# Kernel tuning notes

Measured on AMD Instinct MI355X. Metric: run time of the kernel, lower is better.

Reference implementation:

```python
import jax, jax.numpy as jnp
import numpy as np

TAU_RC = 0.02
TAU_REF = 0.002
V_TH = 1.0
EPS = 1e-7


def lif_rate(I):
    # LIF firing-rate nonlinearity: r = 1/(tau_ref - tau_rc*log1p(-v_th/I)) for I > v_th+eps else 0
    good = I > V_TH + EPS
    safe_I = jnp.where(good, I, V_TH + 1.0)  # avoid log1p of invalid values
    r = 1.0 / (TAU_REF - TAU_RC * jnp.log1p(-V_TH / safe_I))
    return jnp.where(good, r, 0.0)


def setup_inputs() -> dict:
    key = jax.random.key(0)
    kq, kk, kv, ke, kg, kb = jax.random.split(key, 6)
    B, H, T, D = 2, 16, 2048, 64
    block_size = 2048
    Q = jax.random.normal(kq, (B, H, T, D), dtype=jnp.float32)
    K = jax.random.normal(kk, (B, H, T, D), dtype=jnp.float32)
    V = jax.random.normal(kv, (B, H, T, D), dtype=jnp.float32)
    enc = jax.random.normal(ke, (H, block_size, D), dtype=jnp.float32)
    # F.normalize(enc, dim=-1, eps=1e-8): x / max(||x||, eps)
    norm = jnp.maximum(jnp.linalg.norm(enc, axis=-1, keepdims=True), 1e-8)
    enc_hat = enc / norm
    gain = jax.random.uniform(kg, (1, H, block_size, 1), dtype=jnp.float32) * 200.0
    bias = jax.random.uniform(kb, (1, H, block_size, 1), dtype=jnp.float32)
    return {"Q": Q, "K": K, "V": V, "enc_hat": enc_hat, "gain": gain, "bias": bias}


def reference(Q, K, V, enc_hat, gain, bias):
    B, H, T, D = Q.shape
    temperature = jnp.asarray(D ** 0.5, dtype=Q.dtype)
    E = enc_hat[:, :T, :]          # [H, T, D]
    G = gain[:, :, :T, :]          # [1, H, T, 1]
    BIAS = bias[:, :, :T, :]       # [1, H, T, 1]
    # scores against fixed encoders (K is unused, matching the original module)
    I = G * jnp.einsum('bhtd,hsd->bhts', Q, E) + BIAS   # [B, H, T, T]
    scores = lif_rate(I) / temperature
    causal = jnp.tril(jnp.ones((T, T), dtype=bool))[None, None]
    scores = jnp.where(causal, scores, -jnp.inf)
    attn = jax.nn.softmax(scores, axis=-1)
    return jnp.einsum('bhts,bhsd->bhtd', attn, V)
```

## Files before the change

### kernel.cpp

```cpp
#include <hip/hip_runtime.h>
#include <hip/hip_bf16.h>
#include <math.h>

constexpr int Bb = 2, Hh = 16, Tt = 2048;

typedef __attribute__((ext_vector_type(8))) _Float16 f16x8;
typedef __attribute__((ext_vector_type(8))) short bf16x8;
typedef __attribute__((ext_vector_type(4))) float f32x4;
typedef __attribute__((ext_vector_type(16))) float f32x16;
typedef __attribute__((ext_vector_type(4))) unsigned int u32x4;
typedef unsigned int u32;

__device__ __forceinline__ short f2bf(float x){ __hip_bfloat16 h = __float2bfloat16(x); return *(short*)&h; }
__device__ __forceinline__ int swze(int row, int e){ return row*64 + ((((e>>3) ^ (row&7))<<3) | (e&7)); }
__device__ __forceinline__ int swzg(int row, int e0){ return row*64 + ((((e0>>3) ^ (row&7))<<3)); }

__device__ __forceinline__ void gll16(const void* g, void* l){
  __builtin_amdgcn_global_load_lds((const __attribute__((address_space(1))) u32*)g,
                                   (__attribute__((address_space(3))) u32*)l, 16, 0, 0);
}
__device__ __forceinline__ u32 cvtpk(float lo, float hi){
  u32 d; asm("v_cvt_pk_bf16_f32 %0, %1, %2" : "=v"(d) : "v"(lo), "v"(hi)); return d;
}

__global__ __launch_bounds__(256) void prep_e(const float* __restrict__ E, char* __restrict__ Eimg){
  const float* src = E + (size_t)blockIdx.x * 4096;
  char* dst = Eimg + (size_t)blockIdx.x * 16384;
#pragma unroll
  for (int i = 0; i < 2; ++i) {
    const int gid = threadIdx.x + 256 * i;
    const int row = gid >> 3, gc = gid & 7;
    const float* s8 = src + row * 64 + gc * 8;
    float4 a = *(const float4*)s8;
    float4 c = *(const float4*)(s8 + 4);
    float v[8] = {a.x, a.y, a.z, a.w, c.x, c.y, c.z, c.w};
    f16x8 hv, lv;
#pragma unroll
    for (int k = 0; k < 8; ++k) {
      _Float16 hi = (_Float16)v[k];
      hv[k] = hi; lv[k] = (_Float16)(v[k] - (float)hi);
    }
    const int off = row * 128 + ((gc ^ (row & 7)) << 4);
    *(f16x8*)(dst + off) = hv;
    *(f16x8*)(dst + 8192 + off) = lv;
  }
}

__global__ __launch_bounds__(256) void prep_v(const float* __restrict__ V, char* __restrict__ Vimg){
  __shared__ __align__(16) short Tl[64 * 64];
  const int tid = threadIdx.x;
  const int j = blockIdx.x & 31, bh = blockIdx.x >> 5;
  const int s0 = j * 64;
  {
    const int r = tid >> 2, c0 = (tid & 3) * 16;
    const float* src = V + ((size_t)bh * Tt + s0 + r) * 64 + c0;
#pragma unroll
    for (int i = 0; i < 4; ++i) {
      float4 t4 = ((const float4*)src)[i];
      float vv[4] = {t4.x, t4.y, t4.z, t4.w};
#pragma unroll
      for (int k = 0; k < 4; ++k) Tl[swze(c0 + 4 * i + k, r)] = f2bf(vv[k]);
    }
  }
  __syncthreads();
  {
    const int d = tid >> 2, sg = (tid & 3) * 16;
    bf16x8 a = *(const bf16x8*)&Tl[swzg(d, sg)];
    bf16x8 b = *(const bf16x8*)&Tl[swzg(d, sg + 8)];
    char* dst = Vimg + (size_t)blockIdx.x * 8192 + d * 128;
    *(bf16x8*)(dst + ((((sg >> 3) + 0) ^ (d & 7)) << 4)) = a;
    *(bf16x8*)(dst + ((((sg >> 3) + 1) ^ (d & 7)) << 4)) = b;
  }
}

__global__ __launch_bounds__(256, 3) void lif_attn6(
    const float* __restrict__ Q, const float* __restrict__ gain, const float* __restrict__ bias,
    const char* __restrict__ Eimg, const char* __restrict__ Vimg, float* __restrict__ out)
{
  __shared__ __align__(16) char Eb[2][16384];
  __shared__ __align__(16) char Vb[2][8192];
  __shared__ __align__(16) float LsS[128];

  const int tid = threadIdx.x, lane = tid & 63;
  const int l31 = lane & 31, hi2 = lane >> 5;
  const int w = tid >> 6, wc = w & 1, wr = w >> 1;
  const int bh = blockIdx.x & 31, tb = 31 - (blockIdx.x >> 5);
  const int b = bh >> 4, h = bh & 15, t0 = tb * 64;
  const int tg = t0 + 32 * wc + l31;

  const char* etile = Eimg + (size_t)(h * 32) * 16384;
  const char* vtile = Vimg + (size_t)(bh * 32) * 8192;

  f16x8 qh[4], ql[4];
  {
    const float* qp = Q + ((size_t)(b * Hh + h) * Tt + tg) * 64 + 8 * hi2;
#pragma unroll
    for (int kk = 0; kk < 4; ++kk) {
      const float* p0 = qp + 16 * kk;
      float4 a = *(const float4*)p0;
      float4 c = *(const float4*)(p0 + 4);
      float v[8] = {a.x, a.y, a.z, a.w, c.x, c.y, c.z, c.w};
#pragma unroll
      for (int k = 0; k < 8; ++k) {
        _Float16 hi = (_Float16)v[k];
        qh[kk][k] = hi; ql[kk][k] = (_Float16)(v[k] - (float)hi);
      }
    }
  }
  const float gt = gain[h * Tt + tg], bt = bias[h * Tt + tg];

  const int rS = 32 * wr + l31;
  const int eB = rS * 128 + ((hi2 ^ (rS & 7)) << 4);
  const int vB0 = l31 * 128 + (((4 * wr + hi2) ^ (l31 & 7)) << 4);
  const int vB1 = (32 + l31) * 128 + (((4 * wr + hi2) ^ (l31 & 7)) << 4);

  f32x16 oacc0 = 0.f, oacc1 = 0.f;
  float lsum = 0.f;

  {
    const char* g = etile + tid * 16;
#pragma unroll
    for (int c2 = 0; c2 < 4; ++c2) gll16(g + c2 * 4096, &Eb[0][0] + tid * 16 + c2 * 4096);
    const char* gv = vtile + tid * 16;
#pragma unroll
    for (int c2 = 0; c2 < 2; ++c2) gll16(gv + c2 * 4096, &Vb[0][0] + tid * 16 + c2 * 4096);
  }
  __syncthreads();

  int cur = 0;
  for (int j = 0; ; ++j) {
    if (j < tb) {
      const char* g = etile + (size_t)(j + 1) * 16384 + tid * 16;
      char* l = &Eb[cur ^ 1][0] + tid * 16;
#pragma unroll
      for (int c2 = 0; c2 < 4; ++c2) gll16(g + c2 * 4096, l + c2 * 4096);
      const char* gv = vtile + (size_t)(j + 1) * 8192 + tid * 16;
      char* lv = &Vb[cur ^ 1][0] + tid * 16;
#pragma unroll
      for (int c2 = 0; c2 < 2; ++c2) gll16(gv + c2 * 4096, lv + c2 * 4096);
    }
    const char* ec = &Eb[cur][0];
    f32x16 sacc = 0.f;
#pragma unroll
    for (int kk = 0; kk < 4; ++kk) {
      f16x8 eh = *(const f16x8*)(ec + (eB ^ (kk << 5)));
      f16x8 el = *(const f16x8*)(ec + 8192 + (eB ^ (kk << 5)));
      sacc = __builtin_amdgcn_mfma_f32_32x32x16_f16(eh, qh[kk], sacc, 0, 0, 0);
      sacc = __builtin_amdgcn_mfma_f32_32x32x16_f16(el, qh[kk], sacc, 0, 0, 0);
      sacc = __builtin_amdgcn_mfma_f32_32x32x16_f16(eh, ql[kk], sacc, 0, 0, 0);
    }
    float p[16];
#pragma unroll
    for (int r = 0; r < 16; ++r) {
      const float I = fmaf(gt, sacc[r], bt);
      const float L2 = __log2f((I - 1.0f) * __builtin_amdgcn_rcpf(I));
      const float den = fmaf(-0.013862944f, L2, 0.002f);
      const float rd = __builtin_amdgcn_rcpf(den);
      const float pv = __builtin_amdgcn_exp2f(fmaf(0.18033688f, rd, -90.169312f));
      p[r] = (I > 1.0f + 1e-7f) ? pv : 7.1892351e-28f;
    }
    if (j == tb) {
#pragma unroll
      for (int rq = 0; rq < 4; ++rq)
#pragma unroll
        for (int rr = 0; rr < 4; ++rr)
          if (32 * wr + 8 * rq + 4 * hi2 + rr > 32 * wc + l31) p[4 * rq + rr] = 0.f;
    }
#pragma unroll
    for (int r = 0; r < 16; ++r) lsum += p[r];
    const char* vc = &Vb[cur][0];
#pragma unroll
    for (int kp = 0; kp < 2; ++kp) {
      u32 x0 = cvtpk(p[8 * kp + 0], p[8 * kp + 1]);
      u32 x1 = cvtpk(p[8 * kp + 2], p[8 * kp + 3]);
      u32 y0 = cvtpk(p[8 * kp + 4], p[8 * kp + 5]);
      u32 y1 = cvtpk(p[8 * kp + 6], p[8 * kp + 7]);
      asm("v_permlane32_swap_b32 %0, %1" : "+v"(x0), "+v"(y0));
      asm("v_permlane32_swap_b32 %0, %1" : "+v"(x1), "+v"(y1));
      u32x4 af = {x0, x1, y0, y1};
      bf16x8 pa = *(bf16x8*)&af;
      bf16x8 vb0 = *(const bf16x8*)(vc + (vB0 ^ (kp << 5)));
      bf16x8 vb1 = *(const bf16x8*)(vc + (vB1 ^ (kp << 5)));
      oacc0 = __builtin_amdgcn_mfma_f32_32x32x16_bf16(pa, vb0, oacc0, 0, 0, 0);
      oacc1 = __builtin_amdgcn_mfma_f32_32x32x16_bf16(pa, vb1, oacc1, 0, 0, 0);
    }
    if (j == tb) break;
    __syncthreads();
    cur ^= 1;
  }

  lsum += __shfl_xor(lsum, 32);
  if (lane < 32) LsS[wr * 64 + wc * 32 + l31] = lsum;
  __syncthreads();
  float* red = (float*)&Eb[0][0];
  if (wr == 1) {
#pragma unroll
    for (int rq = 0; rq < 4; ++rq)
#pragma unroll
      for (int rr = 0; rr < 4; ++rr) {
        const int tr = 8 * rq + 4 * hi2 + rr;
        red[wc * 2048 + tr * 64 + l31]      = oacc0[4 * rq + rr];
        red[wc * 2048 + tr * 64 + 32 + l31] = oacc1[4 * rq + rr];
      }
  }
  __syncthreads();
  if (wr == 0) {
    float* ob = out + ((size_t)(b * Hh + h) * Tt + t0 + 32 * wc) * 64;
#pragma unroll
    for (int rq = 0; rq < 4; ++rq) {
      const int tr0 = 8 * rq + 4 * hi2;
      f32x4 lt0 = *(const f32x4*)&LsS[wc * 32 + tr0];
      f32x4 lt1 = *(const f32x4*)&LsS[64 + wc * 32 + tr0];
#pragma unroll
      for (int rr = 0; rr < 4; ++rr) {
        const int tr = tr0 + rr;
        const float linv = __builtin_amdgcn_rcpf(lt0[rr] + lt1[rr]);
        const float o0 = oacc0[4 * rq + rr] + red[wc * 2048 + tr * 64 + l31];
        const float o1 = oacc1[4 * rq + rr] + red[wc * 2048 + tr * 64 + 32 + l31];
        ob[(size_t)tr * 64 + l31]      = o0 * linv;
        ob[(size_t)tr * 64 + 32 + l31] = o1 * linv;
      }
    }
  }
}

extern "C" void kernel_launch(void* const* d_in, const int* in_sizes, int n_in,
                              void* d_out, int out_size, void* d_ws, size_t ws_size,
                              hipStream_t stream) {
  const float* Q    = (const float*)d_in[0];
  const float* V    = (const float*)d_in[2];
  const float* E    = (const float*)d_in[3];
  const float* gain = (const float*)d_in[4];
  const float* bias = (const float*)d_in[5];
  float* out = (float*)d_out;

  constexpr size_t EIMG_BYTES = (size_t)Hh * 32 * 16384;
  char* Eimg = (char*)d_ws;
  char* Vimg = (char*)d_ws + EIMG_BYTES;

  prep_e<<<Hh * 32, 256, 0, stream>>>(E, Eimg);
  prep_v<<<Bb * Hh * 32, 256, 0, stream>>>(V, Vimg);
  lif_attn6<<<1024, 256, 0, stream>>>(Q, gain, bias, Eimg, Vimg, out);
}
```

Baseline: 79.36 us.

## Software-pipeline score MFMA one tile ahead and load V directly to registers

Restructures the main loop so the E·Q score MFMAs for tile j+1 run while the LIF transcendental math for tile j executes, with E staged two tiles ahead in a double LDS buffer. V is no longer staged through LDS. prep_v writes a new layout that lets each lane read its bf16x8 B-operand fragments straight from global memory into registers, prefetched one tile ahead. This aims to overlap MFMA with VALU work and cut LDS traffic and footprint, at the cost of more registers (two score accumulators plus V register buffers) under the 3-blocks-per-CU launch bound.

Result: faster. 74.00 us (-6.8%).

```diff
diff --git a/kernel.cpp b/kernel.cpp
--- a/kernel.cpp
+++ b/kernel.cpp
@@ -67,18 +67,17 @@
     const int d = tid >> 2, sg = (tid & 3) * 16;
     bf16x8 a = *(const bf16x8*)&Tl[swzg(d, sg)];
     bf16x8 b = *(const bf16x8*)&Tl[swzg(d, sg + 8)];
-    char* dst = Vimg + (size_t)blockIdx.x * 8192 + d * 128;
-    *(bf16x8*)(dst + ((((sg >> 3) + 0) ^ (d & 7)) << 4)) = a;
-    *(bf16x8*)(dst + ((((sg >> 3) + 1) ^ (d & 7)) << 4)) = b;
-  }
-}
-
-__global__ __launch_bounds__(256, 3) void lif_attn6(
+    char* dst = Vimg + (size_t)blockIdx.x * 8192;
+    *(bf16x8*)(dst + (sg >> 3) * 1024 + d * 16)       = a;
+    *(bf16x8*)(dst + ((sg >> 3) + 1) * 1024 + d * 16) = b;
+  }
+}
+
+__global__ __launch_bounds__(256, 3) void lif_attn8(
     const float* __restrict__ Q, const float* __restrict__ gain, const float* __restrict__ bias,
     const char* __restrict__ Eimg, const char* __restrict__ Vimg, float* __restrict__ out)
 {
   __shared__ __align__(16) char Eb[2][16384];
-  __shared__ __align__(16) char Vb[2][8192];
   __shared__ __align__(16) float LsS[128];
 
   const int tid = threadIdx.x, lane = tid & 63;
@@ -111,48 +110,51 @@
 
   const int rS = 32 * wr + l31;
   const int eB = rS * 128 + ((hi2 ^ (rS & 7)) << 4);
-  const int vB0 = l31 * 128 + (((4 * wr + hi2) ^ (l31 & 7)) << 4);
-  const int vB1 = (32 + l31) * 128 + (((4 * wr + hi2) ^ (l31 & 7)) << 4);
+
+  const int g8a = 4 * wr + hi2;
+  const char* vp0 = vtile + g8a * 1024 + l31 * 16;
+  const char* vp1 = vtile + g8a * 1024 + (32 + l31) * 16;
+  const char* vp2 = vtile + (g8a + 2) * 1024 + l31 * 16;
+  const char* vp3 = vtile + (g8a + 2) * 1024 + (32 + l31) * 16;
 
   f32x16 oacc0 = 0.f, oacc1 = 0.f;
   float lsum = 0.f;
-
-  {
-    const char* g = etile + tid * 16;
-#pragma unroll
-    for (int c2 = 0; c2 < 4; ++c2) gll16(g + c2 * 4096, &Eb[0][0] + tid * 16 + c2 * 4096);
-    const char* gv = vtile + tid * 16;
-#pragma unroll
-    for (int c2 = 0; c2 < 2; ++c2) gll16(gv + c2 * 4096, &Vb[0][0] + tid * 16 + c2 * 4096);
-  }
-  __syncthreads();
-
-  int cur = 0;
-  for (int j = 0; ; ++j) {
-    if (j < tb) {
-      const char* g = etile + (size_t)(j + 1) * 16384 + tid * 16;
-      char* l = &Eb[cur ^ 1][0] + tid * 16;
-#pragma unroll
-      for (int c2 = 0; c2 < 4; ++c2) gll16(g + c2 * 4096, l + c2 * 4096);
-      const char* gv = vtile + (size_t)(j + 1) * 8192 + tid * 16;
-      char* lv = &Vb[cur ^ 1][0] + tid * 16;
-#pragma unroll
-      for (int c2 = 0; c2 < 2; ++c2) gll16(gv + c2 * 4096, lv + c2 * 4096);
-    }
-    const char* ec = &Eb[cur][0];
-    f32x16 sacc = 0.f;
+  f32x16 sA, sB;
+  bf16x8 vA[4], vB[4];
+
+  auto STAGE_E = [&](int n, int buf) {
+    const char* g = etile + (size_t)n * 16384 + tid * 16;
+    char* l = &Eb[buf][0] + tid * 16;
+#pragma unroll
+    for (int c2 = 0; c2 < 4; ++c2) gll16(g + c2 * 4096, l + c2 * 4096);
+  };
+  auto SSTEP = [&](int buf, f32x16& acc) {
+    const char* ec = &Eb[buf][0];
+    acc = 0.f;
 #pragma unroll
     for (int kk = 0; kk < 4; ++kk) {
       f16x8 eh = *(const f16x8*)(ec + (eB ^ (kk << 5)));
       f16x8 el = *(const f16x8*)(ec + 8192 + (eB ^ (kk << 5)));
-      sacc = __builtin_amdgcn_mfma_f32_32x32x16_f16(eh, qh[kk], sacc, 0, 0, 0);
-      sacc = __builtin_amdgcn_mfma_f32_32x32x16_f16(el, qh[kk], sacc, 0, 0, 0);
-      sacc = __builtin_amdgcn_mfma_f32_32x32x16_f16(eh, ql[kk], sacc, 0, 0, 0);
-    }
+      acc = __builtin_amdgcn_mfma_f32_32x32x16_f16(eh, qh[kk], acc, 0, 0, 0);
+      acc = __builtin_amdgcn_mfma_f32_32x32x16_f16(el, qh[kk], acc, 0, 0, 0);
+      acc = __builtin_amdgcn_mfma_f32_32x32x16_f16(eh, ql[kk], acc, 0, 0, 0);
+    }
+  };
+  auto VLOAD = [&](int n, bf16x8* vv) {
+    const size_t o = (size_t)n * 8192;
+    vv[0] = *(const bf16x8*)(vp0 + o);
+    vv[1] = *(const bf16x8*)(vp1 + o);
+    vv[2] = *(const bf16x8*)(vp2 + o);
+    vv[3] = *(const bf16x8*)(vp3 + o);
+  };
+
+  auto BODY = [&](int j, f32x16& cur, f32x16& nxt, bf16x8* vc, bf16x8* vn) {
+    if (j + 2 <= tb) STAGE_E(j + 2, j & 1);
+    if (j + 1 <= tb) { SSTEP((j + 1) & 1, nxt); VLOAD(j + 1, vn); }
     float p[16];
 #pragma unroll
     for (int r = 0; r < 16; ++r) {
-      const float I = fmaf(gt, sacc[r], bt);
+      const float I = fmaf(gt, cur[r], bt);
       const float L2 = __log2f((I - 1.0f) * __builtin_amdgcn_rcpf(I));
       const float den = fmaf(-0.013862944f, L2, 0.002f);
       const float rd = __builtin_amdgcn_rcpf(den);
@@ -168,7 +170,6 @@
     }
 #pragma unroll
     for (int r = 0; r < 16; ++r) lsum += p[r];
-    const char* vc = &Vb[cur][0];
 #pragma unroll
     for (int kp = 0; kp < 2; ++kp) {
       u32 x0 = cvtpk(p[8 * kp + 0], p[8 * kp + 1]);
@@ -179,14 +180,23 @@
       asm("v_permlane32_swap_b32 %0, %1" : "+v"(x1), "+v"(y1));
       u32x4 af = {x0, x1, y0, y1};
       bf16x8 pa = *(bf16x8*)&af;
-      bf16x8 vb0 = *(const bf16x8*)(vc + (vB0 ^ (kp << 5)));
-      bf16x8 vb1 = *(const bf16x8*)(vc + (vB1 ^ (kp << 5)));
-      oacc0 = __builtin_amdgcn_mfma_f32_32x32x16_bf16(pa, vb0, oacc0, 0, 0, 0);
-      oacc1 = __builtin_amdgcn_mfma_f32_32x32x16_bf16(pa, vb1, oacc1, 0, 0, 0);
-    }
-    if (j == tb) break;
+      oacc0 = __builtin_amdgcn_mfma_f32_32x32x16_bf16(pa, vc[2 * kp + 0], oacc0, 0, 0, 0);
+      oacc1 = __builtin_amdgcn_mfma_f32_32x32x16_bf16(pa, vc[2 * kp + 1], oacc1, 0, 0, 0);
+    }
     __syncthreads();
-    cur ^= 1;
+  };
+
+  STAGE_E(0, 0);
+  if (tb >= 1) STAGE_E(1, 1);
+  VLOAD(0, vA);
+  __syncthreads();
+  SSTEP(0, sA);
+  __syncthreads();
+
+  int j = 0;
+  for (;;) {
+    BODY(j, sA, sB, vA, vB); if (j == tb) break; ++j;
+    BODY(j, sB, sA, vB, vA); if (j == tb) break; ++j;
   }
 
   lsum += __shfl_xor(lsum, 32);
@@ -240,5 +250,5 @@
 
   prep_e<<<Hh * 32, 256, 0, stream>>>(E, Eimg);
   prep_v<<<Bb * Hh * 32, 256, 0, stream>>>(V, Vimg);
-  lif_attn6<<<1024, 256, 0, stream>>>(Q, gain, bias, Eimg, Vimg, out);
-}
+  lif_attn8<<<1024, 256, 0, stream>>>(Q, gain, bias, Eimg, Vimg, out);
+}
```
